# Kernel optimization log

Hardware: AMD Instinct MI355X
Metric: run time of the kernel (lower is better)

## Reference

```python
import jax, jax.numpy as jnp
import numpy as np

B, L, D, H, DH, DFF, NL, A = 32, 1024, 512, 8, 64, 2048, 6, 21
CL = 4  # new variables per clique (chain junction tree)


def _build_mask():
    # Mirrors _make_junction_tree_mask: each position attends to itself,
    # to all parent-clique variables, and to earlier vars in its own clique.
    m = np.zeros((L, L), dtype=bool)
    for c in range(L // CL):
        own = range(c * CL, (c + 1) * CL)
        par = range((c - 1) * CL, c * CL) if c > 0 else range(0)
        for i in own:
            m[i, i] = True
            for p in par:
                m[i, p] = True
            for v in own:
                if v < i:
                    m[i, v] = True
    return m


def setup_inputs() -> dict:
    key = jax.random.key(0)
    ks = jax.random.split(key, 12)
    s = 0.02
    inp = {
        "x": jax.random.randint(ks[0], (B, L), 0, A, dtype=jnp.int32),
        "mask": jnp.asarray(_build_mask())[None, None],  # (1,1,L,L), broadcasts over B,H
        "tok_emb": jax.random.normal(ks[1], (A, D)) * s,
        "pos_emb": jax.random.normal(ks[2], (L, D)) * s,
        "wq": jax.random.normal(ks[3], (NL, D, D)) * s,
        "bq": jnp.zeros((NL, D)),
        "wk": jax.random.normal(ks[4], (NL, D, D)) * s,
        "bk": jnp.zeros((NL, D)),
        "wv": jax.random.normal(ks[5], (NL, D, D)) * s,
        "bv": jnp.zeros((NL, D)),
        "wo": jax.random.normal(ks[6], (NL, D, D)) * s,
        "bo": jnp.zeros((NL, D)),
        "ln1_s": jnp.ones((NL, D)),
        "ln1_b": jnp.zeros((NL, D)),
        "ln2_s": jnp.ones((NL, D)),
        "ln2_b": jnp.zeros((NL, D)),
        "w1": jax.random.normal(ks[7], (NL, D, DFF)) * s,
        "b1": jnp.zeros((NL, DFF)),
        "w2": jax.random.normal(ks[8], (NL, DFF, D)) * s,
        "b2": jnp.zeros((NL, D)),
        "wout": jax.random.normal(ks[9], (D, A)) * s,
        "bout": jnp.zeros((A,)),
    }
    return inp


def _ln(x, s, b):
    mu = x.mean(-1, keepdims=True)
    var = ((x - mu) ** 2).mean(-1, keepdims=True)
    return (x - mu) * jax.lax.rsqrt(var + 1e-6) * s + b


def reference(x, mask, tok_emb, pos_emb, wq, bq, wk, bk, wv, bv, wo, bo,
              ln1_s, ln1_b, ln2_s, ln2_b, w1, b1, w2, b2, wout, bout):
    h = tok_emb[x] + pos_emb[None, :, :]           # (B, L, D)
    neg = jnp.asarray(-1e9, h.dtype)
    scale = jnp.asarray(1.0 / np.sqrt(DH), h.dtype)
    for l in range(NL):
        # masked multi-head self-attention (pre-LN block)
        hn = _ln(h, ln1_s[l], ln1_b[l])
        q = (hn @ wq[l] + bq[l]).reshape(B, L, H, DH)
        k = (hn @ wk[l] + bk[l]).reshape(B, L, H, DH)
        v = (hn @ wv[l] + bv[l]).reshape(B, L, H, DH)
        sc = jnp.einsum('blhd,bmhd->bhlm', q, k) * scale
        sc = jnp.where(mask, sc, neg)              # junction-tree sparsity pattern
        attn = jax.nn.softmax(sc, axis=-1)
        o = jnp.einsum('bhlm,bmhd->blhd', attn, v).reshape(B, L, D) @ wo[l] + bo[l]
        h = h + o
        # feed-forward
        hn = _ln(h, ln2_s[l], ln2_b[l])
        h = h + (jax.nn.gelu(hn @ w1[l] + b1[l]) @ w2[l] + b2[l])
    return h @ wout + bout                          # (B, L, alphabet_size)
```

## Files before the change

### kernel.cpp

```cpp
#include <hip/hip_runtime.h>

#define BB 32
#define LL 1024
#define DD 512
#define HH 8
#define DHH 64
#define DFF 2048
#define NLAYERS 6
#define AA 21
#define MTOT (BB*LL)
#define QS 1536

typedef unsigned short u16;
typedef __bf16 bf16x8 __attribute__((ext_vector_type(8)));
typedef float f32x4 __attribute__((ext_vector_type(4)));
typedef u16 u16x8 __attribute__((ext_vector_type(8)));

__device__ __forceinline__ float bf2f(u16 u) {
    return __uint_as_float(((unsigned int)u) << 16);
}
__device__ __forceinline__ u16 f2bf(float f) {
    unsigned int i = __float_as_uint(f);
    unsigned int r = i + 0x7FFFu + ((i >> 16) & 1u);
    return (u16)(r >> 16);
}

__global__ void detect_kernel(const void* __restrict__ tok, int* __restrict__ flag) {
    __shared__ int cnt[256];
    int t = threadIdx.x;
    const u16* p = (const u16*)tok;
    int c = 0;
    #pragma unroll
    for (int j = 0; j < 8; j++) {
        u16 u = p[2 * (t * 8 + j)];
        int e = (u >> 7) & 0xFF;
        c += (e >= 97 && e <= 137) ? 1 : 0;
    }
    cnt[t] = c;
    __syncthreads();
    for (int s = 128; s; s >>= 1) {
        if (t < s) cnt[t] += cnt[t + s];
        __syncthreads();
    }
    if (t == 0) flag[0] = (cnt[0] > 1024) ? 1 : 0;
}

#define NTAB 13
struct ConvTab {
    const void* src[NTAB];
    unsigned long long dstOff[NTAB];
    int n[NTAB];
    int chunk[NTAB];
    int lstride[NTAB];
};
__global__ __launch_bounds__(256) void conv_small(ConvTab tab, u16* __restrict__ spBase,
                                                  const int* __restrict__ flag, int total) {
    int i = blockIdx.x * 256 + threadIdx.x;
    if (i >= total) return;
    int fl = flag[0];
    #pragma unroll 1
    for (int e = 0; e < NTAB; e++) {
        if (i < tab.n[e]) {
            const void* s = tab.src[e];
            u16 val = fl ? ((const u16*)s)[i] : f2bf(((const float*)s)[i]);
            int c = i / tab.chunk[e];
            int r = i - c * tab.chunk[e];
            spBase[tab.dstOff[e] + (size_t)c * tab.lstride[e] + r] = val;
            return;
        }
        i -= tab.n[e];
    }
}

__global__ __launch_bounds__(256) void conv_T(const void* __restrict__ src,
                                              u16* __restrict__ dst, int R, int C,
                                              const int* __restrict__ flag, int dstZS) {
    __shared__ u16 tile[32][33];
    int z = blockIdx.z;
    size_t zoffS = (size_t)z * R * C;
    size_t zoffD = (size_t)z * dstZS;
    int bx = blockIdx.x * 32, by = blockIdx.y * 32;
    int tx = threadIdx.x & 31, ty = threadIdx.x >> 5;
    int fl = flag[0];
    const u16* s16 = (const u16*)src + zoffS;
    const float* s32 = (const float*)src + zoffS;
    #pragma unroll
    for (int r = 0; r < 4; r++) {
        size_t idx = (size_t)(by + ty * 4 + r) * C + bx + tx;
        tile[ty * 4 + r][tx] = fl ? s16[idx] : f2bf(s32[idx]);
    }
    __syncthreads();
    #pragma unroll
    for (int r = 0; r < 4; r++)
        dst[zoffD + (size_t)(bx + ty * 4 + r) * R + by + tx] = tile[tx][ty * 4 + r];
}

__global__ __launch_bounds__(256) void woutpad_kernel(const void* __restrict__ wout,
                                                      const void* __restrict__ bout,
                                                      u16* __restrict__ wpad,
                                                      u16* __restrict__ bpad,
                                                      const int* __restrict__ flag) {
    int i = blockIdx.x * 256 + threadIdx.x;
    int fl = flag[0];
    if (i < 128 * 512) {
        int n = i >> 9, kk = i & 511;
        u16 val = 0;
        if (n < AA) val = fl ? ((const u16*)wout)[kk * AA + n] : f2bf(((const float*)wout)[kk * AA + n]);
        wpad[(size_t)n * 512 + kk] = val;
    }
    if (i < 128) {
        u16 val = 0;
        if (i < AA) val = fl ? ((const u16*)bout)[i] : f2bf(((const float*)bout)[i]);
        bpad[i] = val;
    }
}

__global__ __launch_bounds__(128) void embed_kernel(const int* __restrict__ x,
                                                    const u16* __restrict__ tok_emb,
                                                    const u16* __restrict__ pos_emb,
                                                    u16* __restrict__ h) {
    int row = blockIdx.x;
    int l = row & (LL - 1);
    int tok = x[row];
    int c = threadIdx.x * 4;
    ushort4 te = *(const ushort4*)(tok_emb + (size_t)tok * DD + c);
    ushort4 pe = *(const ushort4*)(pos_emb + (size_t)l * DD + c);
    ushort4 o;
    o.x = f2bf(bf2f(te.x) + bf2f(pe.x));
    o.y = f2bf(bf2f(te.y) + bf2f(pe.y));
    o.z = f2bf(bf2f(te.z) + bf2f(pe.z));
    o.w = f2bf(bf2f(te.w) + bf2f(pe.w));
    *(ushort4*)(h + (size_t)row * DD + c) = o;
}

__global__ __launch_bounds__(256) void ln_kernel(const u16* __restrict__ h,
                                                 const u16* __restrict__ s,
                                                 const u16* __restrict__ b,
                                                 u16* __restrict__ outp) {
    int row = blockIdx.x * 4 + (threadIdx.x >> 6);
    int lane = threadIdx.x & 63;
    u16x8 hv = *(const u16x8*)(h + (size_t)row * DD + lane * 8);
    float v[8];
    #pragma unroll
    for (int i = 0; i < 8; i++) v[i] = bf2f(hv[i]);
    float sum = v[0]+v[1]+v[2]+v[3]+v[4]+v[5]+v[6]+v[7];
    #pragma unroll
    for (int off = 32; off; off >>= 1) sum += __shfl_xor(sum, off, 64);
    float mu = sum * (1.0f / DD);
    float var = 0.f;
    #pragma unroll
    for (int i = 0; i < 8; i++) {
        float d = v[i] - mu;
        var += d * d;
    }
    #pragma unroll
    for (int off = 32; off; off >>= 1) var += __shfl_xor(var, off, 64);
    float rs = rsqrtf(var * (1.0f / DD) + 1e-6f);
    u16x8 sv = *(const u16x8*)(s + lane * 8);
    u16x8 bv = *(const u16x8*)(b + lane * 8);
    u16x8 o;
    #pragma unroll
    for (int i = 0; i < 8; i++)
        o[i] = f2bf((v[i] - mu) * rs * bf2f(sv[i]) + bf2f(bv[i]));
    *(u16x8*)(outp + (size_t)row * DD + lane * 8) = o;
}

#define GLD16(gp, lp) __builtin_amdgcn_global_load_lds( \
    (const __attribute__((address_space(1))) void*)(gp), \
    (__attribute__((address_space(3))) void*)(lp), 16, 0, 0)

template <int EPI>
__global__ __launch_bounds__(256) void gemm_bt(const u16* __restrict__ A,
                                               const u16* __restrict__ BT,
                                               const u16* __restrict__ bias,
                                               u16* __restrict__ Cb,
                                               float* __restrict__ Cf,
                                               int M, int N, int K, int lda,
                                               const int* __restrict__ flag) {
    __shared__ __align__(16) u16 Als[2][128 * 32];
    __shared__ __align__(16) u16 Bls[2][128 * 32];
    const int tid  = threadIdx.x;
    const int lane = tid & 63;
    const int wave = tid >> 6;

    int gx = gridDim.x, gy = gridDim.y;
    int tileX, tileY;
    if ((gy & 7) == 0) {
        int bid = blockIdx.y * gx + blockIdx.x;
        int xcd = bid & 7;
        int idx = bid >> 3;
        int stripe = gy >> 3;
        tileX = idx % gx;
        tileY = xcd * stripe + idx / gx;
    } else {
        tileX = blockIdx.x; tileY = blockIdx.y;
    }
    const int tileM = tileY * 128;
    const int tileN = tileX * 128;
    const int wm = (wave & 1) * 64;
    const int wn = (wave >> 1) * 64;

    const int srow = tid >> 2;
    const int scol = (((tid & 3) ^ ((tid >> 3) & 3))) * 8;

    const u16* Ag0 = A  + (size_t)(tileM + srow) * lda + scol;
    const u16* Ag1 = A  + (size_t)(tileM + 64 + srow) * lda + scol;
    const u16* Bg0 = BT + (size_t)(tileN + srow) * K + scol;
    const u16* Bg1 = BT + (size_t)(tileN + 64 + srow) * K + scol;

    f32x4 acc[4][4] = {};
    const int lm = lane & 15;
    const int lk = (((lane >> 4) ^ ((lm >> 1) & 3))) * 8;

    const int nk = K >> 5;
    GLD16(Ag0, Als[0] + tid * 8);
    GLD16(Ag1, Als[0] + 2048 + tid * 8);
    GLD16(Bg0, Bls[0] + tid * 8);
    GLD16(Bg1, Bls[0] + 2048 + tid * 8);
    __syncthreads();

    for (int kt = 0; kt < nk; kt++) {
        const int cur = kt & 1;
        const int nxt = cur ^ 1;
        if (kt + 1 < nk) {
            const int k1 = (kt + 1) << 5;
            GLD16(Ag0 + k1, Als[nxt] + tid * 8);
            GLD16(Ag1 + k1, Als[nxt] + 2048 + tid * 8);
            GLD16(Bg0 + k1, Bls[nxt] + tid * 8);
            GLD16(Bg1 + k1, Bls[nxt] + 2048 + tid * 8);
        }
        bf16x8 af[4], bfr[4];
        #pragma unroll
        for (int i = 0; i < 4; i++)
            af[i] = *(const bf16x8*)(Als[cur] + (wm + i * 16 + lm) * 32 + lk);
        #pragma unroll
        for (int j = 0; j < 4; j++)
            bfr[j] = *(const bf16x8*)(Bls[cur] + (wn + j * 16 + lm) * 32 + lk);
        #pragma unroll
        for (int i = 0; i < 4; i++)
            #pragma unroll
            for (int j = 0; j < 4; j++)
                acc[i][j] = __builtin_amdgcn_mfma_f32_16x16x32_bf16(af[i], bfr[j], acc[i][j], 0, 0, 0);
        __syncthreads();
    }

    int fl = 0;
    if constexpr (EPI == 3) fl = flag[0];
    const u16* Hb = (const u16*)Cf;
    const int r0 = (lane >> 4) * 4;
    #pragma unroll
    for (int j = 0; j < 4; j++) {
        int col = tileN + wn + j * 16 + lm;
        float bv = bf2f(bias[col]);
        #pragma unroll
        for (int i = 0; i < 4; i++) {
            int row = tileM + wm + i * 16 + r0;
            #pragma unroll
            for (int r = 0; r < 4; r++) {
                float xv = acc[i][j][r] + bv;
                if constexpr (EPI == 0) {
                    Cb[(size_t)(row + r) * N + col] = f2bf(xv);
                } else if constexpr (EPI == 1) {
                    float u = 1.5957691216057308f * (xv + 0.044715f * xv * xv * xv);
                    float t = 1.0f - 2.0f / (__expf(u) + 1.0f);
                    Cb[(size_t)(row + r) * N + col] = f2bf(0.5f * xv * (1.0f + t));
                } else if constexpr (EPI == 2) {
                    size_t idx = (size_t)(row + r) * N + col;
                    Cb[idx] = f2bf(bf2f(Cb[idx]) + xv);
                } else if constexpr (EPI == 4) {
                    size_t idx = (size_t)(row + r) * N + col;
                    Cb[idx] = f2bf(xv + bf2f(Hb[idx]));
                } else {
                    if (col < AA) {
                        size_t idx = (size_t)(row + r) * AA + col;
                        if (fl) Cb[idx] = f2bf(xv);
                        else    Cf[idx] = xv;
                    }
                }
            }
        }
    }
}

__global__ __launch_bounds__(256) void attn_kernel(u16* qkv) {
    int bl   = blockIdx.x * 4 + (threadIdx.x >> 6);
    int lane = threadIdx.x & 63;
    int l    = bl & (LL - 1);
    int lo   = (l & ~3) - 4; if (lo < 0) lo = 0;
    int nj   = l - lo + 1;

    size_t qrow = (size_t)bl * QS;
    int off = lane * 8;

    u16x8 q8 = *(const u16x8*)(qkv + qrow + off);
    float qf[8];
    #pragma unroll
    for (int i = 0; i < 8; i++) qf[i] = bf2f(q8[i]) * 0.125f;

    size_t base = (size_t)(bl - (l - lo)) * QS;
    float sc[8];
    u16x8 v8[8];
    #pragma unroll
    for (int j = 0; j < 8; j++) {
        int jc = (j < nj) ? j : (nj - 1);
        const u16* krow = qkv + base + (size_t)jc * QS;
        u16x8 k8 = *(const u16x8*)(krow + 512 + off);
        v8[j]    = *(const u16x8*)(krow + 1024 + off);
        float t = 0.f;
        #pragma unroll
        for (int i = 0; i < 8; i++) t = fmaf(qf[i], bf2f(k8[i]), t);
        t += __shfl_xor(t, 1, 64);
        t += __shfl_xor(t, 2, 64);
        t += __shfl_xor(t, 4, 64);
        sc[j] = (j < nj) ? t : -1e30f;
    }
    float m = sc[0];
    #pragma unroll
    for (int j = 1; j < 8; j++) m = fmaxf(m, sc[j]);
    float p[8], den = 0.f;
    #pragma unroll
    for (int j = 0; j < 8; j++) { p[j] = __expf(sc[j] - m); den += p[j]; }
    float inv = 1.0f / den;
    float o[8] = {};
    #pragma unroll
    for (int j = 0; j < 8; j++)
        #pragma unroll
        for (int i = 0; i < 8; i++) o[i] = fmaf(p[j], bf2f(v8[j][i]), o[i]);
    u16x8 ov;
    #pragma unroll
    for (int i = 0; i < 8; i++) ov[i] = f2bf(o[i] * inv);
    *(u16x8*)(qkv + qrow + off) = ov;
}

extern "C" void kernel_launch(void* const* d_in, const int* in_sizes, int n_in,
                              void* d_out, int out_size, void* d_ws, size_t ws_size,
                              hipStream_t stream) {
    const int base = n_in - 22;
    const int*  x    = (const int*)d_in[0];
    const void* tokI = d_in[2 + base];
    const void* posI = d_in[3 + base];
    const void* wqI  = d_in[4 + base];
    const void* bqI  = d_in[5 + base];
    const void* wkI  = d_in[6 + base];
    const void* bkI  = d_in[7 + base];
    const void* wvI  = d_in[8 + base];
    const void* bvI  = d_in[9 + base];
    const void* woI  = d_in[10 + base];
    const void* boI  = d_in[11 + base];
    const void* ln1sI = d_in[12 + base];
    const void* ln1bI = d_in[13 + base];
    const void* ln2sI = d_in[14 + base];
    const void* ln2bI = d_in[15 + base];
    const void* w1I  = d_in[16 + base];
    const void* b1I  = d_in[17 + base];
    const void* w2I  = d_in[18 + base];
    const void* b2I  = d_in[19 + base];
    const void* woutI = d_in[20 + base];
    const void* boutI = d_in[21 + base];

    char* ws = (char*)d_ws;
    u16*  h    = (u16*)(ws + 0);
    u16*  hn   = (u16*)(ws + 67108864);
    u16*  qkv  = (u16*)(ws + 100663296);
    u16*  wT   = (u16*)(ws + 201326592);
    u16*  sp   = (u16*)(ws + 239075328);
    int* flag  = (int*)(ws + 240500736);

    u16* mid = qkv;

    u16* wqkvT = wT;
    u16* woT   = wT + 4718592;
    u16* w1T   = wT + 6291456;
    u16* w2T   = wT + 12582912;

    const unsigned long long oWoutPad = 0;
    const unsigned long long oBoutPad = 65536;
    const unsigned long long oTok     = 65664;
    const unsigned long long oPos     = 76416;
    const unsigned long long oQkvB    = 600704;
    const unsigned long long oBo      = 609920;
    const unsigned long long oB1      = 612992;
    const unsigned long long oB2      = 625280;
    const unsigned long long oLn1s    = 628352;
    const unsigned long long oLn1b    = 631424;
    const unsigned long long oLn2s    = 634496;
    const unsigned long long oLn2b    = 637568;

    detect_kernel<<<1, 256, 0, stream>>>(tokI, flag);

    ConvTab tab;
    const void* srcs[NTAB] = {tokI, bqI, bkI, bvI, boI, b1I, b2I, ln1sI, ln1bI, ln2sI, ln2bI, posI, tokI};
    unsigned long long offs[NTAB] = {oTok, oQkvB, oQkvB + 512, oQkvB + 1024, oBo, oB1, oB2,
                                     oLn1s, oLn1b, oLn2s, oLn2b, oPos, oTok};
    int ns[NTAB]     = {10752, 3072, 3072, 3072, 3072, 12288, 3072, 3072, 3072, 3072, 3072, 524288, 0};
    int chunks[NTAB] = {10752, 512, 512, 512, 3072, 12288, 3072, 3072, 3072, 3072, 3072, 524288, 1};
    int lstr[NTAB]   = {10752, 1536, 1536, 1536, 3072, 12288, 3072, 3072, 3072, 3072, 3072, 524288, 1};
    int total = 0;
    for (int e = 0; e < NTAB; e++) {
        tab.src[e] = srcs[e]; tab.dstOff[e] = offs[e]; tab.n[e] = ns[e];
        tab.chunk[e] = chunks[e]; tab.lstride[e] = lstr[e];
        total += ns[e];
    }
    conv_small<<<(total + 255) / 256, 256, 0, stream>>>(tab, sp, flag, total);
    woutpad_kernel<<<256, 256, 0, stream>>>(woutI, boutI, sp + oWoutPad, sp + oBoutPad, flag);

    conv_T<<<dim3(16, 16, 6), 256, 0, stream>>>(wqI, wqkvT,          DD, DD, flag, 786432);
    conv_T<<<dim3(16, 16, 6), 256, 0, stream>>>(wkI, wqkvT + 262144, DD, DD, flag, 786432);
    conv_T<<<dim3(16, 16, 6), 256, 0, stream>>>(wvI, wqkvT + 524288, DD, DD, flag, 786432);
    conv_T<<<dim3(16, 16, 6), 256, 0, stream>>>(woI, woT, DD, DD, flag, 262144);
    conv_T<<<dim3(64, 16, 6), 256, 0, stream>>>(w1I, w1T, DD, DFF, flag, 1048576);
    conv_T<<<dim3(16, 64, 6), 256, 0, stream>>>(w2I, w2T, DFF, DD, flag, 1048576);

    embed_kernel<<<MTOT, 128, 0, stream>>>(x, sp + oTok, sp + oPos, h);

    for (int l = 0; l < NLAYERS; l++) {
        u16* wqkvTl = wqkvT + (size_t)l * 786432;
        u16* woTl   = woT + (size_t)l * 262144;
        u16* w1Tl   = w1T + (size_t)l * 1048576;
        u16* w2Tl   = w2T + (size_t)l * 1048576;

        ln_kernel<<<MTOT / 4, 256, 0, stream>>>(h, sp + oLn1s + l * DD, sp + oLn1b + l * DD, hn);

        gemm_bt<0><<<dim3(QS / 128, MTOT / 128), 256, 0, stream>>>(
            hn, wqkvTl, sp + oQkvB + l * QS, qkv, nullptr, MTOT, QS, DD, DD, flag);

        attn_kernel<<<MTOT / 4, 256, 0, stream>>>(qkv);

        gemm_bt<2><<<dim3(DD / 128, MTOT / 128), 256, 0, stream>>>(
            qkv, woTl, sp + oBo + l * DD, h, nullptr, MTOT, DD, DD, QS, flag);

        ln_kernel<<<MTOT / 4, 256, 0, stream>>>(h, sp + oLn2s + l * DD, sp + oLn2b + l * DD, hn);

        for (int half = 0; half < 2; half++) {
            const u16* Ahn = hn + (size_t)half * 16384 * DD;
            u16* hHalf = h + (size_t)half * 16384 * DD;
            gemm_bt<1><<<dim3(DFF / 128, 16384 / 128), 256, 0, stream>>>(
                Ahn, w1Tl, sp + oB1 + l * DFF, mid, nullptr, 16384, DFF, DD, DD, flag);
            if (l < NLAYERS - 1) {
                gemm_bt<2><<<dim3(DD / 128, 16384 / 128), 256, 0, stream>>>(
                    mid, w2Tl, sp + oB2 + l * DD, hHalf, nullptr, 16384, DD, DFF, DFF, flag);
            } else {
                gemm_bt<4><<<dim3(DD / 128, 16384 / 128), 256, 0, stream>>>(
                    mid, w2Tl, sp + oB2 + l * DD, hn + (size_t)half * 16384 * DD, (float*)hHalf,
                    16384, DD, DFF, DFF, flag);
            }
        }
    }

    gemm_bt<3><<<dim3(1, MTOT / 128), 256, 0, stream>>>(
        hn, sp + oWoutPad, sp + oBoutPad, (u16*)d_out, (float*)d_out, MTOT, 128, DD, DD, flag);
}
```

Baseline: 2.629 ms.

## Process a whole clique per wave in attention and merge the FFN halves

The attention kernel now assigns one wavefront to a clique of 4 query rows. It loads the 8 shared K/V rows once and reuses them for all 4 queries, instead of reloading them for every query, which cuts K/V global traffic in attention. The FFN GEMMs are also launched once over all rows instead of in two halves. To make room for the full-size intermediate buffer, hn and qkv move to new workspace offsets. This raises per-thread register use in attention and roughly doubles the size of the mid buffer.

```diff
diff --git a/kernel.cpp b/kernel.cpp
--- a/kernel.cpp
+++ b/kernel.cpp
@@ -283,53 +283,59 @@
 }
 
 __global__ __launch_bounds__(256) void attn_kernel(u16* qkv) {
-    int bl   = blockIdx.x * 4 + (threadIdx.x >> 6);
+    int g    = blockIdx.x * 4 + (threadIdx.x >> 6);
     int lane = threadIdx.x & 63;
-    int l    = bl & (LL - 1);
-    int lo   = (l & ~3) - 4; if (lo < 0) lo = 0;
-    int nj   = l - lo + 1;
-
-    size_t qrow = (size_t)bl * QS;
+    int c    = g & 255;
+    int lo   = (c == 0) ? 0 : c * 4 - 4;
+    int nbase = c * 4 - lo;
+    size_t rowQ0 = (size_t)(g >> 8) * LL + c * 4;
+    size_t rowK0 = (size_t)(g >> 8) * LL + lo;
     int off = lane * 8;
 
-    u16x8 q8 = *(const u16x8*)(qkv + qrow + off);
-    float qf[8];
-    #pragma unroll
-    for (int i = 0; i < 8; i++) qf[i] = bf2f(q8[i]) * 0.125f;
-
-    size_t base = (size_t)(bl - (l - lo)) * QS;
-    float sc[8];
-    u16x8 v8[8];
+    u16x8 k8[8], v8[8];
     #pragma unroll
     for (int j = 0; j < 8; j++) {
-        int jc = (j < nj) ? j : (nj - 1);
-        const u16* krow = qkv + base + (size_t)jc * QS;
-        u16x8 k8 = *(const u16x8*)(krow + 512 + off);
-        v8[j]    = *(const u16x8*)(krow + 1024 + off);
-        float t = 0.f;
-        #pragma unroll
-        for (int i = 0; i < 8; i++) t = fmaf(qf[i], bf2f(k8[i]), t);
-        t += __shfl_xor(t, 1, 64);
-        t += __shfl_xor(t, 2, 64);
-        t += __shfl_xor(t, 4, 64);
-        sc[j] = (j < nj) ? t : -1e30f;
-    }
-    float m = sc[0];
-    #pragma unroll
-    for (int j = 1; j < 8; j++) m = fmaxf(m, sc[j]);
-    float p[8], den = 0.f;
-    #pragma unroll
-    for (int j = 0; j < 8; j++) { p[j] = __expf(sc[j] - m); den += p[j]; }
-    float inv = 1.0f / den;
-    float o[8] = {};
-    #pragma unroll
-    for (int j = 0; j < 8; j++)
-        #pragma unroll
-        for (int i = 0; i < 8; i++) o[i] = fmaf(p[j], bf2f(v8[j][i]), o[i]);
-    u16x8 ov;
-    #pragma unroll
-    for (int i = 0; i < 8; i++) ov[i] = f2bf(o[i] * inv);
-    *(u16x8*)(qkv + qrow + off) = ov;
+        const u16* krow = qkv + (rowK0 + j) * QS;
+        k8[j] = *(const u16x8*)(krow + 512 + off);
+        v8[j] = *(const u16x8*)(krow + 1024 + off);
+    }
+
+    #pragma unroll
+    for (int q = 0; q < 4; q++) {
+        int nj = nbase + q + 1;
+        size_t qrow = (rowQ0 + q) * QS;
+        u16x8 q8 = *(const u16x8*)(qkv + qrow + off);
+        float qf[8];
+        #pragma unroll
+        for (int i = 0; i < 8; i++) qf[i] = bf2f(q8[i]) * 0.125f;
+        float sc[8];
+        #pragma unroll
+        for (int j = 0; j < 8; j++) {
+            float t = 0.f;
+            #pragma unroll
+            for (int i = 0; i < 8; i++) t = fmaf(qf[i], bf2f(k8[j][i]), t);
+            t += __shfl_xor(t, 1, 64);
+            t += __shfl_xor(t, 2, 64);
+            t += __shfl_xor(t, 4, 64);
+            sc[j] = (j < nj) ? t : -1e30f;
+        }
+        float m = sc[0];
+        #pragma unroll
+        for (int j = 1; j < 8; j++) m = fmaxf(m, sc[j]);
+        float p[8], den = 0.f;
+        #pragma unroll
+        for (int j = 0; j < 8; j++) { p[j] = __expf(sc[j] - m); den += p[j]; }
+        float inv = 1.0f / den;
+        float o[8] = {};
+        #pragma unroll
+        for (int j = 0; j < 8; j++)
+            #pragma unroll
+            for (int i = 0; i < 8; i++) o[i] = fmaf(p[j], bf2f(v8[j][i]), o[i]);
+        u16x8 ov;
+        #pragma unroll
+        for (int i = 0; i < 8; i++) ov[i] = f2bf(o[i] * inv);
+        *(u16x8*)(qkv + qrow + off) = ov;
+    }
 }
 
 extern "C" void kernel_launch(void* const* d_in, const int* in_sizes, int n_in,
@@ -360,8 +366,8 @@
 
     char* ws = (char*)d_ws;
     u16*  h    = (u16*)(ws + 0);
-    u16*  hn   = (u16*)(ws + 67108864);
-    u16*  qkv  = (u16*)(ws + 100663296);
+    u16*  hn   = (u16*)(ws + 33554432);
+    u16*  qkv  = (u16*)(ws + 67108864);
     u16*  wT   = (u16*)(ws + 201326592);
     u16*  sp   = (u16*)(ws + 239075328);
     int* flag  = (int*)(ws + 240500736);
@@ -424,26 +430,21 @@
         gemm_bt<0><<<dim3(QS / 128, MTOT / 128), 256, 0, stream>>>(
             hn, wqkvTl, sp + oQkvB + l * QS, qkv, nullptr, MTOT, QS, DD, DD, flag);
 
-        attn_kernel<<<MTOT / 4, 256, 0, stream>>>(qkv);
+        attn_kernel<<<MTOT / 16, 256, 0, stream>>>(qkv);
 
         gemm_bt<2><<<dim3(DD / 128, MTOT / 128), 256, 0, stream>>>(
             qkv, woTl, sp + oBo + l * DD, h, nullptr, MTOT, DD, DD, QS, flag);
 
         ln_kernel<<<MTOT / 4, 256, 0, stream>>>(h, sp + oLn2s + l * DD, sp + oLn2b + l * DD, hn);
 
-        for (int half = 0; half < 2; half++) {
-            const u16* Ahn = hn + (size_t)half * 16384 * DD;
-            u16* hHalf = h + (size_t)half * 16384 * DD;
-            gemm_bt<1><<<dim3(DFF / 128, 16384 / 128), 256, 0, stream>>>(
-                Ahn, w1Tl, sp + oB1 + l * DFF, mid, nullptr, 16384, DFF, DD, DD, flag);
-            if (l < NLAYERS - 1) {
-                gemm_bt<2><<<dim3(DD / 128, 16384 / 128), 256, 0, stream>>>(
-                    mid, w2Tl, sp + oB2 + l * DD, hHalf, nullptr, 16384, DD, DFF, DFF, flag);
-            } else {
-                gemm_bt<4><<<dim3(DD / 128, 16384 / 128), 256, 0, stream>>>(
-                    mid, w2Tl, sp + oB2 + l * DD, hn + (size_t)half * 16384 * DD, (float*)hHalf,
-                    16384, DD, DFF, DFF, flag);
-            }
+        gemm_bt<1><<<dim3(DFF / 128, MTOT / 128), 256, 0, stream>>>(
+            hn, w1Tl, sp + oB1 + l * DFF, mid, nullptr, MTOT, DFF, DD, DD, flag);
+        if (l < NLAYERS - 1) {
+            gemm_bt<2><<<dim3(DD / 128, MTOT / 128), 256, 0, stream>>>(
+                mid, w2Tl, sp + oB2 + l * DD, h, nullptr, MTOT, DD, DFF, DFF, flag);
+        } else {
+            gemm_bt<4><<<dim3(DD / 128, MTOT / 128), 256, 0, stream>>>(
+                mid, w2Tl, sp + oB2 + l * DD, hn, (float*)h, MTOT, DD, DFF, DFF, flag);
         }
     }
 
```

Measured after the change: 2.546 ms (median of 2 runs). 3.1% less time.
